# Kernel optimization log

Measured on AMD Instinct MI355X. Metric: run time of the kernel, lower is better.

Reference implementation:

```python
import jax, jax.numpy as jnp
import numpy as np

DISTANCE_WEIGHT = 1.001  # self.distence_weight in the torch module


def setup_inputs() -> dict:
    key = jax.random.key(0)
    k1, k2 = jax.random.split(key)
    B, DIM_IN, DIM_OUT = 1024, 512, 512
    x = jax.random.normal(k1, (B, DIM_IN), dtype=jnp.float32)
    centers = jax.random.normal(k2, (DIM_OUT, DIM_IN), dtype=jnp.float32)
    beta = jnp.ones((DIM_OUT,), dtype=jnp.float32)
    return {"x": x, "centers": centers, "beta": beta}


def reference(x, centers, beta):
    # L1 pairwise distance: [B, dim_out]
    sim = jnp.sum(jnp.abs(x[:, None, :] - centers[None, :, :]), axis=-1)
    # negate, shift by global max * distance_weight, scale by beta
    sim = -sim + jnp.max(sim) * DISTANCE_WEIGHT
    return beta * sim
```

## Files before the change

kernel.cpp:

```cpp
#include <hip/hip_runtime.h>


typedef _Float16 h2 __attribute__((ext_vector_type(2)));
typedef float f4 __attribute__((ext_vector_type(4)));
typedef unsigned int u32;
typedef unsigned int u32x4 __attribute__((ext_vector_type(4)));

#define DIM_O 512
#define DIM_K 512
#define W_DIST 1.001f

__device__ __forceinline__ h2 as_h2(u32 u){ h2 r; __builtin_memcpy(&r,&u,4); return r; }
__device__ __forceinline__ u32 as_u(h2 h){ u32 r; __builtin_memcpy(&r,&h,4); return r; }
__device__ __forceinline__ u32 cvt2(float a, float b){
    auto h = __builtin_amdgcn_cvt_pkrtz(a, b);
    u32 r; __builtin_memcpy(&r, &h, 4); return r;
}

__global__ __launch_bounds__(64) void k_sim(const float* __restrict__ X,
                                            const float* __restrict__ C,
                                            float* __restrict__ S,
                                            float* __restrict__ bmax)
{
    __shared__ __align__(16) char lds[6144];
    const int tid = threadIdx.x;
    const int bx = blockIdx.x & 15;
    const int by = blockIdx.x >> 4;
    const int row0 = by * 16, col0 = bx * 32;
    const int tr = tid >> 4;
    const int tc = tid & 15;

    const float* xsrc = X + (row0 + (tid & 15)) * DIM_K + (tid >> 4) * 8;
    const float* csrc = C + (col0 + (tid & 31)) * DIM_K + (tid >> 5) * 8;
    char* xdst = lds + tid * 16;
    char* cdst = lds + 2048 + tid * 16;

    f4 xv[4], cv[8];
    auto loadc = [&](int t) {
        const float* xq = xsrc + t * 64;
        const float* cq = csrc + t * 64;
#pragma unroll
        for (int i = 0; i < 2; ++i)
#pragma unroll
            for (int h = 0; h < 2; ++h)
                xv[2 * i + h] = *(const f4*)(xq + i * 32 + h * 4);
#pragma unroll
        for (int i = 0; i < 4; ++i)
#pragma unroll
            for (int h = 0; h < 2; ++h)
                cv[2 * i + h] = *(const f4*)(cq + i * 16 + h * 4);
    };

    float acc[4][2] = {};
    const h2 one2 = {(_Float16)1.f, (_Float16)1.f};

    loadc(0);

    for (int t = 0; t < 8; ++t) {
#pragma unroll
        for (int i = 0; i < 2; ++i) {
            u32x4 w;
            w[0] = cvt2(xv[2 * i].x,     xv[2 * i].y);
            w[1] = cvt2(xv[2 * i].z,     xv[2 * i].w);
            w[2] = cvt2(xv[2 * i + 1].x, xv[2 * i + 1].y);
            w[3] = cvt2(xv[2 * i + 1].z, xv[2 * i + 1].w);
            *(u32x4*)(xdst + i * 1024) = w;
        }
#pragma unroll
        for (int i = 0; i < 4; ++i) {
            u32x4 w;
            w[0] = cvt2(cv[2 * i].x,     cv[2 * i].y);
            w[1] = cvt2(cv[2 * i].z,     cv[2 * i].w);
            w[2] = cvt2(cv[2 * i + 1].x, cv[2 * i + 1].y);
            w[3] = cvt2(cv[2 * i + 1].z, cv[2 * i + 1].w);
            *(u32x4*)(cdst + i * 1024) = w;
        }
        if (t < 7) loadc(t + 1);

#pragma unroll
        for (int g = 0; g < 8; ++g) {
            const int xo = (g >> 2) * 1024 + (g & 3) * 256 + tr * 64;
            const int co = 2048 + (g >> 1) * 1024 + (g & 1) * 512 + tc * 16;
            u32x4 xr[4], cr[2];
            xr[0] = *(const u32x4*)(lds + xo);
            xr[1] = *(const u32x4*)(lds + xo + 16);
            xr[2] = *(const u32x4*)(lds + xo + 32);
            xr[3] = *(const u32x4*)(lds + xo + 48);
            cr[0] = *(const u32x4*)(lds + co);
            cr[1] = *(const u32x4*)(lds + co + 256);
#pragma unroll
            for (int k2 = 0; k2 < 4; ++k2) {
#pragma unroll
                for (int i = 0; i < 4; ++i) {
                    h2 a = as_h2(xr[i][k2]);
#pragma unroll
                    for (int j = 0; j < 2; ++j) {
                        h2 d = a - as_h2(cr[j][k2]);
                        h2 ad = as_h2(as_u(d) & 0x7fff7fffu);
                        acc[i][j] = __builtin_amdgcn_fdot2(ad, one2, acc[i][j], false);
                    }
                }
            }
        }
    }

    float m = 0.f;
#pragma unroll
    for (int i = 0; i < 4; ++i) {
        const int r = row0 + tr * 4 + i;
        S[r * DIM_O + col0 + tc]      = acc[i][0];
        S[r * DIM_O + col0 + tc + 16] = acc[i][1];
        m = fmaxf(m, fmaxf(acc[i][0], acc[i][1]));
    }
#pragma unroll
    for (int off = 32; off > 0; off >>= 1)
        m = fmaxf(m, __shfl_xor(m, off, 64));
    if (tid == 0) bmax[blockIdx.x] = m;
}

__global__ __launch_bounds__(256) void k_out(float* __restrict__ S,
                                             const float* __restrict__ beta,
                                             const float* __restrict__ bmax)
{
    const int tid = threadIdx.x;
    const int lane = tid & 63;
    float m = 0.f;
#pragma unroll
    for (int i = 0; i < 16; ++i)
        m = fmaxf(m, bmax[lane + 64 * i]);
#pragma unroll
    for (int off = 32; off > 0; off >>= 1)
        m = fmaxf(m, __shfl_xor(m, off, 64));
    const float shift = m * W_DIST;

    const int f = blockIdx.x * 256 + tid;
    f4 s = ((const f4*)S)[f];
    f4 b = ((const f4*)beta)[f & 127];
    f4 r;
    r.x = b.x * (shift - s.x);
    r.y = b.y * (shift - s.y);
    r.z = b.z * (shift - s.z);
    r.w = b.w * (shift - s.w);
    ((f4*)S)[f] = r;
}

extern "C" void kernel_launch(void* const* d_in, const int* in_sizes, int n_in,
                              void* d_out, int out_size, void* d_ws, size_t ws_size,
                              hipStream_t stream) {
    const float* X = (const float*)d_in[0];
    const float* C = (const float*)d_in[1];
    const float* beta = (const float*)d_in[2];
    float* S = (float*)d_out;
    float* bmax = (float*)d_ws;
    k_sim<<<1024, 64, 0, stream>>>(X, C, S, bmax);
    k_out<<<512, 256, 0, stream>>>(S, beta, bmax);
}
```

Before: 80.40 us.

## Fuse distance and output kernels via cooperative grid sync

Merges the two kernels into one cooperative launch. Each block keeps its accumulators in registers, publishes its block max, waits at a grid-wide barrier, then reads all block maxima and writes the final beta-scaled output directly. This removes the second launch and the write-then-reread of the intermediate matrix. In exchange it pays for a grid sync across 1024 blocks, which depends on all blocks being co-resident.

```diff
diff --git a/kernel.cpp b/kernel.cpp
--- a/kernel.cpp
+++ b/kernel.cpp
@@ -1,5 +1,8 @@
 #include <hip/hip_runtime.h>
+#include <hip/hip_cooperative_groups.h>
 
+
+namespace cg = cooperative_groups;
 
 typedef _Float16 h2 __attribute__((ext_vector_type(2)));
 typedef float f4 __attribute__((ext_vector_type(4)));
@@ -17,10 +20,11 @@
     u32 r; __builtin_memcpy(&r, &h, 4); return r;
 }
 
-__global__ __launch_bounds__(64) void k_sim(const float* __restrict__ X,
-                                            const float* __restrict__ C,
-                                            float* __restrict__ S,
-                                            float* __restrict__ bmax)
+__global__ __launch_bounds__(64) void k_fused(const float* __restrict__ X,
+                                              const float* __restrict__ C,
+                                              const float* __restrict__ beta,
+                                              float* __restrict__ O,
+                                              float* __restrict__ bmax)
 {
     __shared__ __align__(16) char lds[6144];
     const int tid = threadIdx.x;
@@ -106,42 +110,34 @@
 
     float m = 0.f;
 #pragma unroll
-    for (int i = 0; i < 4; ++i) {
-        const int r = row0 + tr * 4 + i;
-        S[r * DIM_O + col0 + tc]      = acc[i][0];
-        S[r * DIM_O + col0 + tc + 16] = acc[i][1];
+    for (int i = 0; i < 4; ++i)
         m = fmaxf(m, fmaxf(acc[i][0], acc[i][1]));
-    }
 #pragma unroll
     for (int off = 32; off > 0; off >>= 1)
         m = fmaxf(m, __shfl_xor(m, off, 64));
     if (tid == 0) bmax[blockIdx.x] = m;
-}
 
-__global__ __launch_bounds__(256) void k_out(float* __restrict__ S,
-                                             const float* __restrict__ beta,
-                                             const float* __restrict__ bmax)
-{
-    const int tid = threadIdx.x;
-    const int lane = tid & 63;
-    float m = 0.f;
+    const float b0 = beta[col0 + tc];
+    const float b1 = beta[col0 + tc + 16];
+
+    __threadfence();
+    cg::this_grid().sync();
+
+    float gm = 0.f;
 #pragma unroll
     for (int i = 0; i < 16; ++i)
-        m = fmaxf(m, bmax[lane + 64 * i]);
+        gm = fmaxf(gm, bmax[tid + 64 * i]);
 #pragma unroll
     for (int off = 32; off > 0; off >>= 1)
-        m = fmaxf(m, __shfl_xor(m, off, 64));
-    const float shift = m * W_DIST;
+        gm = fmaxf(gm, __shfl_xor(gm, off, 64));
+    const float shift = gm * W_DIST;
 
-    const int f = blockIdx.x * 256 + tid;
-    f4 s = ((const f4*)S)[f];
-    f4 b = ((const f4*)beta)[f & 127];
-    f4 r;
-    r.x = b.x * (shift - s.x);
-    r.y = b.y * (shift - s.y);
-    r.z = b.z * (shift - s.z);
-    r.w = b.w * (shift - s.w);
-    ((f4*)S)[f] = r;
+#pragma unroll
+    for (int i = 0; i < 4; ++i) {
+        const int r = row0 + tr * 4 + i;
+        O[r * DIM_O + col0 + tc]      = b0 * (shift - acc[i][0]);
+        O[r * DIM_O + col0 + tc + 16] = b1 * (shift - acc[i][1]);
+    }
 }
 
 extern "C" void kernel_launch(void* const* d_in, const int* in_sizes, int n_in,
@@ -150,8 +146,8 @@
     const float* X = (const float*)d_in[0];
     const float* C = (const float*)d_in[1];
     const float* beta = (const float*)d_in[2];
-    float* S = (float*)d_out;
+    float* O = (float*)d_out;
     float* bmax = (float*)d_ws;
-    k_sim<<<1024, 64, 0, stream>>>(X, C, S, bmax);
-    k_out<<<512, 256, 0, stream>>>(S, beta, bmax);
+    void* args[] = {(void*)&X, (void*)&C, (void*)&beta, (void*)&O, (void*)&bmax};
+    hipLaunchCooperativeKernel((void*)k_fused, dim3(1024), dim3(64), args, 0, stream);
 }
```

Result: slower. 142.7 us (+77.5%).
